# Kernel tuning notes

Hardware: AMD Instinct MI355X
Metric: run time of the kernel (lower is better)

Reference implementation:

```python
import jax, jax.numpy as jnp
import numpy as np

# Config mirrors cfg['cluster'] and point_cloud_range from init_kwargs
PCR = np.array([-51.2, -51.2, -5.0, 51.2, 51.2, 3.0], dtype=np.float32)
VOXEL_SIZE = 0.2
SIZE_X = 512  # floor((51.2 - (-51.2)) / 0.2)
EPS = 1.5
MIN_SAMPLES = 5
MIN_P_CLUSTER = 20


def _cluster(points):
    """Faithful jax version of Cluster.forward for batch_size == 1.

    voxel_down_sample -> DBSCAN (euclidean, eps, min_samples) on voxel coords
    -> drop clusters with < MIN_P_CLUSTER voxels -> scatter labels back to points.
    """
    N = points.shape[0]
    # --- voxel_down_sample ---
    coords = jnp.floor((points[:, 1:3] - PCR[:2]) / VOXEL_SIZE).astype(jnp.int32)  # (N,2) x,y
    merged = coords[:, 1] * SIZE_X + coords[:, 0]
    # static-size unique: padded entries get fill_value=-1 at the end
    uniq, inv = jnp.unique(merged, size=N, fill_value=-1, return_inverse=True)
    valid = uniq >= 0  # (N,) real voxels
    vox = jnp.stack([uniq % SIZE_X, uniq // SIZE_X], axis=1).astype(jnp.float32)  # (N,2)

    # --- DBSCAN on voxel coords ---
    d2 = jnp.sum((vox[:, None, :] - vox[None, :, :]) ** 2, axis=-1)  # (N,N)
    adj = (d2 <= EPS * EPS) & valid[:, None] & valid[None, :]  # includes self-edge
    core = (jnp.sum(adj, axis=1) >= MIN_SAMPLES) & valid  # sklearn counts self

    BIG = N  # sentinel > any label
    labels0 = jnp.where(core, jnp.arange(N), BIG)
    adj_core = adj & core[None, :]

    def min_core_neighbor(labels):
        return jnp.min(jnp.where(adj_core, labels[None, :], BIG), axis=1)

    def body(carry):
        labels, _ = carry
        new = jnp.where(core, jnp.minimum(labels, min_core_neighbor(labels)), labels)
        return new, jnp.any(new != labels)

    # min-label propagation = connected components over core-core eps graph
    labels, _ = jax.lax.while_loop(lambda c: c[1], body, (labels0, jnp.array(True)))

    # border points attach to a neighboring core cluster; otherwise noise (-1)
    nb = min_core_neighbor(labels)
    raw = jnp.where(core, labels, jnp.where(valid & (nb < BIG), nb, -1))  # root-id or -1

    # relabel root-ids to consecutive 0..k-1 (sklearn numbering by smallest core idx)
    roots = jnp.unique(raw, size=N, fill_value=BIG)  # sorted; BIG padding at end
    pos = jnp.searchsorted(roots, raw)
    dense = pos - (roots[0] == -1).astype(pos.dtype)
    dense = jnp.where(raw >= 0, dense, -1)

    # drop small clusters (by voxel count), keep remaining ids unchanged
    counts = jnp.zeros(N, jnp.int32).at[jnp.where(dense >= 0, dense, 0)].add(
        jnp.where(dense >= 0, 1, 0))
    keep = counts >= MIN_P_CLUSTER
    final = jnp.where((dense >= 0) & keep[jnp.clip(dense, 0, N - 1)], dense, -1)

    # scatter voxel labels back to points (points_inst_idx has points.dtype, like torch)
    pts_inst = final[inv].astype(points.dtype)
    max_num_inst = jnp.maximum(jnp.max(final) + 1, 0)
    return pts_inst, max_num_inst


def setup_inputs() -> dict:
    key = jax.random.key(0)
    N = 8192
    k1, k2, k3, k4, k5, k6, k7 = jax.random.split(key, 7)
    n_blobs = 64
    centers = jax.random.uniform(k1, (n_blobs, 2), minval=-48.0, maxval=48.0)
    assign = jax.random.randint(k2, (N,), 0, n_blobs)
    xy = centers[assign] + jax.random.normal(k3, (N, 2)) * 1.0
    noise = jax.random.uniform(k4, (N,)) < 0.2
    xy = jnp.where(noise[:, None], jax.random.uniform(k5, (N, 2), minval=-51.0, maxval=51.0), xy)
    xy = jnp.clip(xy, -51.0, 51.0)
    z = jax.random.uniform(k6, (N, 1), minval=-3.0, maxval=1.0)
    feat = jax.random.normal(k7, (N, 1))
    points = jnp.concatenate([jnp.zeros((N, 1)), xy, z, feat], axis=1).astype(jnp.float32)
    return {"points": points, "batch_size": 1}


def reference(points, batch_size):
    # voxel_down_sample asserts batch_size == 1; single-batch path.
    return _cluster(points)
```

## Files before the change

kernel.cpp:

```cpp
#include <hip/hip_runtime.h>
#include <stdint.h>


#define GRIDW 512
#define WPR 16
#define NWORDS 8192
#define NCELLS 262144
#define NONE 0xFFFFFFFFu

#define OFF_OCC    0
#define OFF_ROOTBM 8192
#define OFF_KEEPBM 16384
#define OFF_RPRE   24576
#define OFF_LAB    32768
#define OFF_CNT    294912

__device__ __forceinline__ void hsum(uint32_t l, uint32_t c, uint32_t r,
                                     uint32_t& h0, uint32_t& h1) {
  uint32_t Wb = (c << 1) | (l >> 31);
  uint32_t Eb = (c >> 1) | (r << 31);
  h0 = Wb ^ c ^ Eb;
  h1 = (Wb & c) | (Eb & (Wb ^ c));
}

__device__ __forceinline__ uint32_t ge5(uint32_t a0, uint32_t a1, uint32_t b0,
                                        uint32_t b1, uint32_t c0, uint32_t c1) {
  uint32_t u0 = a0 ^ b0, cy = a0 & b0;
  uint32_t t = a1 ^ b1;
  uint32_t u1 = t ^ cy;
  uint32_t u2 = (a1 & b1) | (cy & t);
  uint32_t v0 = u0 ^ c0, k0 = u0 & c0;
  uint32_t t2 = u1 ^ c1;
  uint32_t v1 = t2 ^ k0;
  uint32_t k1 = (u1 & c1) | (k0 & t2);
  uint32_t v2 = u2 ^ k1;
  uint32_t v3 = u2 & k1;
  return v3 | (v2 & (v1 | v0));
}

__device__ __forceinline__ uint32_t coreRbit(uint32_t cU, uint32_t rU, uint32_t cM,
                                             uint32_t rM, uint32_t cD, uint32_t rD) {
  if (!(rM & 1u)) return 0u;
  int n = __popc((cU >> 31) | ((rU & 3u) << 1)) +
          __popc((cM >> 31) | ((rM & 3u) << 1)) +
          __popc((cD >> 31) | ((rD & 3u) << 1));
  return n >= 5 ? 1u : 0u;
}

__device__ __forceinline__ uint32_t coreLbit(uint32_t cU, uint32_t lU, uint32_t cM,
                                             uint32_t lM, uint32_t cD, uint32_t lD) {
  if (!(lM >> 31)) return 0u;
  int n = __popc(((lU >> 30) & 3u) | ((cU & 1u) << 2)) +
          __popc(((lM >> 30) & 3u) | ((cM & 1u) << 2)) +
          __popc(((lD >> 30) & 3u) | ((cD & 1u) << 2));
  return n >= 5 ? 1u : 0u;
}

__device__ __forceinline__ uint32_t aread(uint32_t* p) {
  return __hip_atomic_load(p, __ATOMIC_RELAXED, __HIP_MEMORY_SCOPE_AGENT);
}

__device__ __forceinline__ uint32_t findc(uint32_t* L, uint32_t x) {
  uint32_t r = x, p = aread(&L[r]);
  while (p != r) { r = p; p = aread(&L[r]); }
  while (x > r) {
    uint32_t nx = aread(&L[x]);
    if (nx <= r) break;
    atomicCAS(&L[x], nx, r);
    x = nx;
  }
  return r;
}

__device__ __forceinline__ void unite(uint32_t* L, uint32_t a, uint32_t b) {
  for (;;) {
    a = findc(L, a);
    b = findc(L, b);
    if (a == b) return;
    uint32_t lo = min(a, b), hi = max(a, b);
    if (atomicCAS(&L[hi], hi, lo) == hi) return;
    a = lo; b = hi;
  }
}

__global__ void k_init(uint32_t* __restrict__ ws) {
  int i = blockIdx.x * 256 + threadIdx.x;
  ws[OFF_LAB + i] = (uint32_t)i;
  ws[OFF_CNT + i] = 0u;
  if (i < NWORDS) { ws[OFF_OCC + i] = 0u; ws[OFF_ROOTBM + i] = 0u; }
}

__global__ void k_vox(const float* __restrict__ pts, uint32_t* __restrict__ ws,
                      int npts) {
  int i = blockIdx.x * 256 + threadIdx.x;
  if (i >= npts) return;
  float x = pts[i * 5 + 1];
  float y = pts[i * 5 + 2];
  int cx = (int)floorf((x - (-51.2f)) / 0.2f);
  int cy = (int)floorf((y - (-51.2f)) / 0.2f);
  cx = min(max(cx, 0), GRIDW - 1);
  cy = min(max(cy, 0), GRIDW - 1);
  int cell = cy * GRIDW + cx;
  atomicOr(&ws[OFF_OCC + (cell >> 5)], 1u << (cell & 31));
}

__global__ void k_merge(uint32_t* __restrict__ ws) {
  int cell = blockIdx.x * 256 + threadIdx.x;
  const uint32_t* occ = ws + OFF_OCC;
  uint32_t* lab = ws + OFF_LAB;
  int wi = cell >> 5, b = cell & 31, wx = wi & 15, y = cell >> 9;
  uint32_t cB = occ[wi];
  if (!((cB >> b) & 1)) return;
  uint32_t lB = wx ? occ[wi - 1] : 0u;
  uint32_t rB = (wx < 15) ? occ[wi + 1] : 0u;
  uint32_t cA = 0, lA = 0, rA = 0, cC = 0, lC = 0, rC = 0, cD = 0, lD = 0, rD = 0;
  if (y > 0) { int w = wi - WPR; cA = occ[w]; lA = wx ? occ[w - 1] : 0u; rA = (wx < 15) ? occ[w + 1] : 0u; }
  if (y < GRIDW - 1) { int w = wi + WPR; cC = occ[w]; lC = wx ? occ[w - 1] : 0u; rC = (wx < 15) ? occ[w + 1] : 0u; }
  if (y < GRIDW - 2) { int w = wi + 2 * WPR; cD = occ[w]; lD = wx ? occ[w - 1] : 0u; rD = (wx < 15) ? occ[w + 1] : 0u; }
  uint32_t hA0, hA1, hB0, hB1, hC0, hC1, hD0, hD1;
  hsum(lA, cA, rA, hA0, hA1); hsum(lB, cB, rB, hB0, hB1);
  hsum(lC, cC, rC, hC0, hC1); hsum(lD, cD, rD, hD0, hD1);
  uint32_t cmB = ge5(hA0, hA1, hB0, hB1, hC0, hC1) & cB;
  if (!((cmB >> b) & 1)) return;
  bool eC = (b < 31) ? (((cmB >> (b + 1)) & 1) != 0)
                     : (coreRbit(cA, rA, cB, rB, cC, rC) != 0);
  if (eC) unite(lab, cell, cell + 1);
  if (y < GRIDW - 1) {
    uint32_t cmS = ge5(hB0, hB1, hC0, hC1, hD0, hD1) & cC;
    if ((cmS >> b) & 1) unite(lab, cell, cell + GRIDW);
    bool seC = (b < 31) ? (((cmS >> (b + 1)) & 1) != 0)
                        : (coreRbit(cB, rB, cC, rC, cD, rD) != 0);
    if (seC) unite(lab, cell, cell + GRIDW + 1);
    bool swC = (b > 0) ? (((cmS >> (b - 1)) & 1) != 0)
                       : (coreLbit(cB, lB, cC, lC, cD, lD) != 0);
    if (swC) unite(lab, cell, cell + GRIDW - 1);
  }
}

__global__ void k_cb(uint32_t* __restrict__ ws) {
  int cell = blockIdx.x * 256 + threadIdx.x;
  const uint32_t* occ = ws + OFF_OCC;
  uint32_t* lab = ws + OFF_LAB;
  uint32_t* cnt = ws + OFF_CNT;
  int wi = cell >> 5, b = cell & 31, wx = wi & 15, y = cell >> 9;
  uint32_t cB = occ[wi];
  if (!((cB >> b) & 1)) return;
  uint32_t lB = wx ? occ[wi - 1] : 0u;
  uint32_t rB = (wx < 15) ? occ[wi + 1] : 0u;
  uint32_t cZ = 0, lZ = 0, rZ = 0, cA = 0, lA = 0, rA = 0;
  uint32_t cC = 0, lC = 0, rC = 0, cD = 0, lD = 0, rD = 0;
  if (y > 1) { int w = wi - 2 * WPR; cZ = occ[w]; lZ = wx ? occ[w - 1] : 0u; rZ = (wx < 15) ? occ[w + 1] : 0u; }
  if (y > 0) { int w = wi - WPR; cA = occ[w]; lA = wx ? occ[w - 1] : 0u; rA = (wx < 15) ? occ[w + 1] : 0u; }
  if (y < GRIDW - 1) { int w = wi + WPR; cC = occ[w]; lC = wx ? occ[w - 1] : 0u; rC = (wx < 15) ? occ[w + 1] : 0u; }
  if (y < GRIDW - 2) { int w = wi + 2 * WPR; cD = occ[w]; lD = wx ? occ[w - 1] : 0u; rD = (wx < 15) ? occ[w + 1] : 0u; }
  uint32_t hZ0, hZ1, hA0, hA1, hB0, hB1, hC0, hC1, hD0, hD1;
  hsum(lZ, cZ, rZ, hZ0, hZ1); hsum(lA, cA, rA, hA0, hA1); hsum(lB, cB, rB, hB0, hB1);
  hsum(lC, cC, rC, hC0, hC1); hsum(lD, cD, rD, hD0, hD1);
  uint32_t cw0 = ge5(hA0, hA1, hB0, hB1, hC0, hC1) & cB;
  if ((cw0 >> b) & 1) {
    uint32_t root = findc(lab, cell);
    lab[cell] = root;
    if (root == (uint32_t)cell) atomicOr(&ws[OFF_ROOTBM + wi], 1u << b);
    atomicAdd(&cnt[root], 1u);
  } else {
    uint32_t cwm1 = ge5(hZ0, hZ1, hA0, hA1, hB0, hB1) & cA;
    uint32_t cw1 = ge5(hB0, hB1, hC0, hC1, hD0, hD1) & cC;
    uint32_t m = NONE;
    bool t;
    t = (b > 0) ? (((cw0 >> (b - 1)) & 1) != 0) : (coreLbit(cA, lA, cB, lB, cC, lC) != 0);
    if (t) m = min(m, findc(lab, cell - 1));
    t = (b < 31) ? (((cw0 >> (b + 1)) & 1) != 0) : (coreRbit(cA, rA, cB, rB, cC, rC) != 0);
    if (t) m = min(m, findc(lab, cell + 1));
    if (y > 0) {
      if ((cwm1 >> b) & 1) m = min(m, findc(lab, cell - GRIDW));
      t = (b > 0) ? (((cwm1 >> (b - 1)) & 1) != 0) : (coreLbit(cZ, lZ, cA, lA, cB, lB) != 0);
      if (t) m = min(m, findc(lab, cell - GRIDW - 1));
      t = (b < 31) ? (((cwm1 >> (b + 1)) & 1) != 0) : (coreRbit(cZ, rZ, cA, rA, cB, rB) != 0);
      if (t) m = min(m, findc(lab, cell - GRIDW + 1));
    }
    if (y < GRIDW - 1) {
      if ((cw1 >> b) & 1) m = min(m, findc(lab, cell + GRIDW));
      t = (b > 0) ? (((cw1 >> (b - 1)) & 1) != 0) : (coreLbit(cB, lB, cC, lC, cD, lD) != 0);
      if (t) m = min(m, findc(lab, cell + GRIDW - 1));
      t = (b < 31) ? (((cw1 >> (b + 1)) & 1) != 0) : (coreRbit(cB, rB, cC, rC, cD, rD) != 0);
      if (t) m = min(m, findc(lab, cell + GRIDW + 1));
    }
    lab[cell] = m;
    if (m != NONE) atomicAdd(&cnt[m], 1u);
  }
}

__global__ void k_finish(uint32_t* __restrict__ ws, float* __restrict__ out,
                         int npts) {
  __shared__ uint32_t wsum[4];
  __shared__ int smax;
  int tid = threadIdx.x;
  if (tid == 0) smax = -1;
  int base = tid * 32;
  uint32_t s = 0;
  for (int j = 0; j < 32; j++) s += __popc(ws[OFF_ROOTBM + base + j]);
  int lane = tid & 63, wv = tid >> 6;
  uint32_t inc = s;
  for (int d = 1; d < 64; d <<= 1) { uint32_t t = __shfl_up(inc, d); if (lane >= d) inc += t; }
  if (lane == 63) wsum[wv] = inc;
  __syncthreads();
  uint32_t woff = 0;
  for (int k = 0; k < wv; k++) woff += wsum[k];
  uint32_t excl = woff + inc - s;
  int mx = -1;
  for (int j = 0; j < 32; j++) {
    uint32_t rbw = ws[OFF_ROOTBM + base + j];
    ws[OFF_RPRE + base + j] = excl;
    uint32_t rb = rbw, keep = 0;
    int d = (int)excl;
    while (rb) {
      int b2 = __ffs(rb) - 1; rb &= rb - 1;
      int r = (base + j) * 32 + b2;
      if (ws[OFF_CNT + r] >= 20u) { keep |= 1u << b2; mx = d; }
      d++;
    }
    ws[OFF_KEEPBM + base + j] = keep;
    excl += __popc(rbw);
  }
  if (mx >= 0) atomicMax(&smax, mx);
  __syncthreads();
  if (tid == 0) out[npts] = (float)(smax + 1);
}

__global__ void k_scatter(const float* __restrict__ pts,
                          const uint32_t* __restrict__ ws,
                          float* __restrict__ out, int npts) {
  int i = blockIdx.x * 256 + threadIdx.x;
  if (i >= npts) return;
  float x = pts[i * 5 + 1];
  float y = pts[i * 5 + 2];
  int cx = (int)floorf((x - (-51.2f)) / 0.2f);
  int cy = (int)floorf((y - (-51.2f)) / 0.2f);
  cx = min(max(cx, 0), GRIDW - 1);
  cy = min(max(cy, 0), GRIDW - 1);
  int cell = cy * GRIDW + cx;
  uint32_t l = ws[OFF_LAB + cell];
  float o = -1.0f;
  if (l != NONE) {
    if ((ws[OFF_KEEPBM + (l >> 5)] >> (l & 31)) & 1) {
      int dnum = ws[OFF_RPRE + (l >> 5)] +
                 __popc(ws[OFF_ROOTBM + (l >> 5)] & ((1u << (l & 31)) - 1u));
      o = (float)dnum;
    }
  }
  out[i] = o;
}

extern "C" void kernel_launch(void* const* d_in, const int* in_sizes, int n_in,
                              void* d_out, int out_size, void* d_ws, size_t ws_size,
                              hipStream_t stream) {
  const float* pts = (const float*)d_in[0];
  int npts = in_sizes[0] / 5;
  uint32_t* ws = (uint32_t*)d_ws;
  float* out = (float*)d_out;
  int pblocks = (npts + 255) / 256;
  k_init<<<NCELLS / 256, 256, 0, stream>>>(ws);
  k_vox<<<pblocks, 256, 0, stream>>>(pts, ws, npts);
  k_merge<<<NCELLS / 256, 256, 0, stream>>>(ws);
  k_cb<<<NCELLS / 256, 256, 0, stream>>>(ws);
  k_finish<<<1, 256, 0, stream>>>(ws, out, npts);
  k_scatter<<<pblocks, 256, 0, stream>>>(pts, ws, out, npts);
}
```

Measured before the change: 113.7 us.

## Build a compact worklist of occupied voxels and drop the full-grid init kernel

Voxelization now appends each newly occupied cell to a compact worklist and lazily initializes that cell's label and count. This replaces the full-grid init kernel with a small memset of the occupancy bitmap, root bitmap and worklist counter. The merge and core/border kernels launch a fixed 32 blocks over the worklist instead of one thread per grid cell, and fetch the extra neighbor rows (Z and D) only on the branches that need them. This removes dense-grid traffic and idle threads. The fixed 32×256 grid assumes at most 8192 occupied cells, and worklist order is no longer spatial, so memory access becomes less coalesced.

```diff
diff --git a/kernel.cpp b/kernel.cpp
--- a/kernel.cpp
+++ b/kernel.cpp
@@ -5,15 +5,17 @@
 #define GRIDW 512
 #define WPR 16
 #define NWORDS 8192
-#define NCELLS 262144
 #define NONE 0xFFFFFFFFu
 
 #define OFF_OCC    0
 #define OFF_ROOTBM 8192
-#define OFF_KEEPBM 16384
-#define OFF_RPRE   24576
-#define OFF_LAB    32768
-#define OFF_CNT    294912
+#define OFF_NOCC   16384
+#define FILL_BYTES ((16384 + 1) * 4)
+#define OFF_WL     16448
+#define OFF_KEEPBM 24640
+#define OFF_RPRE   32832
+#define OFF_LAB    41024
+#define OFF_CNT    303168
 
 __device__ __forceinline__ void hsum(uint32_t l, uint32_t c, uint32_t r,
                                      uint32_t& h0, uint32_t& h1) {
@@ -83,13 +85,6 @@
   }
 }
 
-__global__ void k_init(uint32_t* __restrict__ ws) {
-  int i = blockIdx.x * 256 + threadIdx.x;
-  ws[OFF_LAB + i] = (uint32_t)i;
-  ws[OFF_CNT + i] = 0u;
-  if (i < NWORDS) { ws[OFF_OCC + i] = 0u; ws[OFF_ROOTBM + i] = 0u; }
-}
-
 __global__ void k_vox(const float* __restrict__ pts, uint32_t* __restrict__ ws,
                       int npts) {
   int i = blockIdx.x * 256 + threadIdx.x;
@@ -101,31 +96,40 @@
   cx = min(max(cx, 0), GRIDW - 1);
   cy = min(max(cy, 0), GRIDW - 1);
   int cell = cy * GRIDW + cx;
-  atomicOr(&ws[OFF_OCC + (cell >> 5)], 1u << (cell & 31));
+  uint32_t old = atomicOr(&ws[OFF_OCC + (cell >> 5)], 1u << (cell & 31));
+  if (!((old >> (cell & 31)) & 1)) {
+    uint32_t idx = atomicAdd(&ws[OFF_NOCC], 1u);
+    ws[OFF_WL + idx] = (uint32_t)cell;
+    ws[OFF_LAB + cell] = (uint32_t)cell;
+    ws[OFF_CNT + cell] = 0u;
+  }
 }
 
 __global__ void k_merge(uint32_t* __restrict__ ws) {
-  int cell = blockIdx.x * 256 + threadIdx.x;
+  int i = blockIdx.x * 256 + threadIdx.x;
+  if (i >= (int)ws[OFF_NOCC]) return;
+  int cell = (int)ws[OFF_WL + i];
   const uint32_t* occ = ws + OFF_OCC;
   uint32_t* lab = ws + OFF_LAB;
   int wi = cell >> 5, b = cell & 31, wx = wi & 15, y = cell >> 9;
   uint32_t cB = occ[wi];
-  if (!((cB >> b) & 1)) return;
   uint32_t lB = wx ? occ[wi - 1] : 0u;
   uint32_t rB = (wx < 15) ? occ[wi + 1] : 0u;
-  uint32_t cA = 0, lA = 0, rA = 0, cC = 0, lC = 0, rC = 0, cD = 0, lD = 0, rD = 0;
+  uint32_t cA = 0, lA = 0, rA = 0, cC = 0, lC = 0, rC = 0;
   if (y > 0) { int w = wi - WPR; cA = occ[w]; lA = wx ? occ[w - 1] : 0u; rA = (wx < 15) ? occ[w + 1] : 0u; }
   if (y < GRIDW - 1) { int w = wi + WPR; cC = occ[w]; lC = wx ? occ[w - 1] : 0u; rC = (wx < 15) ? occ[w + 1] : 0u; }
-  if (y < GRIDW - 2) { int w = wi + 2 * WPR; cD = occ[w]; lD = wx ? occ[w - 1] : 0u; rD = (wx < 15) ? occ[w + 1] : 0u; }
-  uint32_t hA0, hA1, hB0, hB1, hC0, hC1, hD0, hD1;
-  hsum(lA, cA, rA, hA0, hA1); hsum(lB, cB, rB, hB0, hB1);
-  hsum(lC, cC, rC, hC0, hC1); hsum(lD, cD, rD, hD0, hD1);
+  uint32_t hA0, hA1, hB0, hB1, hC0, hC1;
+  hsum(lA, cA, rA, hA0, hA1); hsum(lB, cB, rB, hB0, hB1); hsum(lC, cC, rC, hC0, hC1);
   uint32_t cmB = ge5(hA0, hA1, hB0, hB1, hC0, hC1) & cB;
   if (!((cmB >> b) & 1)) return;
   bool eC = (b < 31) ? (((cmB >> (b + 1)) & 1) != 0)
                      : (coreRbit(cA, rA, cB, rB, cC, rC) != 0);
   if (eC) unite(lab, cell, cell + 1);
   if (y < GRIDW - 1) {
+    uint32_t cD = 0, lD = 0, rD = 0;
+    if (y < GRIDW - 2) { int w = wi + 2 * WPR; cD = occ[w]; lD = wx ? occ[w - 1] : 0u; rD = (wx < 15) ? occ[w + 1] : 0u; }
+    uint32_t hD0, hD1;
+    hsum(lD, cD, rD, hD0, hD1);
     uint32_t cmS = ge5(hB0, hB1, hC0, hC1, hD0, hD1) & cC;
     if ((cmS >> b) & 1) unite(lab, cell, cell + GRIDW);
     bool seC = (b < 31) ? (((cmS >> (b + 1)) & 1) != 0)
@@ -138,24 +142,21 @@
 }
 
 __global__ void k_cb(uint32_t* __restrict__ ws) {
-  int cell = blockIdx.x * 256 + threadIdx.x;
+  int i = blockIdx.x * 256 + threadIdx.x;
+  if (i >= (int)ws[OFF_NOCC]) return;
+  int cell = (int)ws[OFF_WL + i];
   const uint32_t* occ = ws + OFF_OCC;
   uint32_t* lab = ws + OFF_LAB;
   uint32_t* cnt = ws + OFF_CNT;
   int wi = cell >> 5, b = cell & 31, wx = wi & 15, y = cell >> 9;
   uint32_t cB = occ[wi];
-  if (!((cB >> b) & 1)) return;
   uint32_t lB = wx ? occ[wi - 1] : 0u;
   uint32_t rB = (wx < 15) ? occ[wi + 1] : 0u;
-  uint32_t cZ = 0, lZ = 0, rZ = 0, cA = 0, lA = 0, rA = 0;
-  uint32_t cC = 0, lC = 0, rC = 0, cD = 0, lD = 0, rD = 0;
-  if (y > 1) { int w = wi - 2 * WPR; cZ = occ[w]; lZ = wx ? occ[w - 1] : 0u; rZ = (wx < 15) ? occ[w + 1] : 0u; }
+  uint32_t cA = 0, lA = 0, rA = 0, cC = 0, lC = 0, rC = 0;
   if (y > 0) { int w = wi - WPR; cA = occ[w]; lA = wx ? occ[w - 1] : 0u; rA = (wx < 15) ? occ[w + 1] : 0u; }
   if (y < GRIDW - 1) { int w = wi + WPR; cC = occ[w]; lC = wx ? occ[w - 1] : 0u; rC = (wx < 15) ? occ[w + 1] : 0u; }
-  if (y < GRIDW - 2) { int w = wi + 2 * WPR; cD = occ[w]; lD = wx ? occ[w - 1] : 0u; rD = (wx < 15) ? occ[w + 1] : 0u; }
-  uint32_t hZ0, hZ1, hA0, hA1, hB0, hB1, hC0, hC1, hD0, hD1;
-  hsum(lZ, cZ, rZ, hZ0, hZ1); hsum(lA, cA, rA, hA0, hA1); hsum(lB, cB, rB, hB0, hB1);
-  hsum(lC, cC, rC, hC0, hC1); hsum(lD, cD, rD, hD0, hD1);
+  uint32_t hA0, hA1, hB0, hB1, hC0, hC1;
+  hsum(lA, cA, rA, hA0, hA1); hsum(lB, cB, rB, hB0, hB1); hsum(lC, cC, rC, hC0, hC1);
   uint32_t cw0 = ge5(hA0, hA1, hB0, hB1, hC0, hC1) & cB;
   if ((cw0 >> b) & 1) {
     uint32_t root = findc(lab, cell);
@@ -163,8 +164,6 @@
     if (root == (uint32_t)cell) atomicOr(&ws[OFF_ROOTBM + wi], 1u << b);
     atomicAdd(&cnt[root], 1u);
   } else {
-    uint32_t cwm1 = ge5(hZ0, hZ1, hA0, hA1, hB0, hB1) & cA;
-    uint32_t cw1 = ge5(hB0, hB1, hC0, hC1, hD0, hD1) & cC;
     uint32_t m = NONE;
     bool t;
     t = (b > 0) ? (((cw0 >> (b - 1)) & 1) != 0) : (coreLbit(cA, lA, cB, lB, cC, lC) != 0);
@@ -172,6 +171,11 @@
     t = (b < 31) ? (((cw0 >> (b + 1)) & 1) != 0) : (coreRbit(cA, rA, cB, rB, cC, rC) != 0);
     if (t) m = min(m, findc(lab, cell + 1));
     if (y > 0) {
+      uint32_t cZ = 0, lZ = 0, rZ = 0;
+      if (y > 1) { int w = wi - 2 * WPR; cZ = occ[w]; lZ = wx ? occ[w - 1] : 0u; rZ = (wx < 15) ? occ[w + 1] : 0u; }
+      uint32_t hZ0, hZ1;
+      hsum(lZ, cZ, rZ, hZ0, hZ1);
+      uint32_t cwm1 = ge5(hZ0, hZ1, hA0, hA1, hB0, hB1) & cA;
       if ((cwm1 >> b) & 1) m = min(m, findc(lab, cell - GRIDW));
       t = (b > 0) ? (((cwm1 >> (b - 1)) & 1) != 0) : (coreLbit(cZ, lZ, cA, lA, cB, lB) != 0);
       if (t) m = min(m, findc(lab, cell - GRIDW - 1));
@@ -179,6 +183,11 @@
       if (t) m = min(m, findc(lab, cell - GRIDW + 1));
     }
     if (y < GRIDW - 1) {
+      uint32_t cD = 0, lD = 0, rD = 0;
+      if (y < GRIDW - 2) { int w = wi + 2 * WPR; cD = occ[w]; lD = wx ? occ[w - 1] : 0u; rD = (wx < 15) ? occ[w + 1] : 0u; }
+      uint32_t hD0, hD1;
+      hsum(lD, cD, rD, hD0, hD1);
+      uint32_t cw1 = ge5(hB0, hB1, hC0, hC1, hD0, hD1) & cC;
       if ((cw1 >> b) & 1) m = min(m, findc(lab, cell + GRIDW));
       t = (b > 0) ? (((cw1 >> (b - 1)) & 1) != 0) : (coreLbit(cB, lB, cC, lC, cD, lD) != 0);
       if (t) m = min(m, findc(lab, cell + GRIDW - 1));
@@ -241,12 +250,10 @@
   int cell = cy * GRIDW + cx;
   uint32_t l = ws[OFF_LAB + cell];
   float o = -1.0f;
-  if (l != NONE) {
-    if ((ws[OFF_KEEPBM + (l >> 5)] >> (l & 31)) & 1) {
-      int dnum = ws[OFF_RPRE + (l >> 5)] +
-                 __popc(ws[OFF_ROOTBM + (l >> 5)] & ((1u << (l & 31)) - 1u));
-      o = (float)dnum;
-    }
+  if (l != NONE && ((ws[OFF_KEEPBM + (l >> 5)] >> (l & 31)) & 1)) {
+    int dnum = ws[OFF_RPRE + (l >> 5)] +
+               __popc(ws[OFF_ROOTBM + (l >> 5)] & ((1u << (l & 31)) - 1u));
+    o = (float)dnum;
   }
   out[i] = o;
 }
@@ -259,10 +266,10 @@
   uint32_t* ws = (uint32_t*)d_ws;
   float* out = (float*)d_out;
   int pblocks = (npts + 255) / 256;
-  k_init<<<NCELLS / 256, 256, 0, stream>>>(ws);
+  hipMemsetAsync(d_ws, 0, FILL_BYTES, stream);
   k_vox<<<pblocks, 256, 0, stream>>>(pts, ws, npts);
-  k_merge<<<NCELLS / 256, 256, 0, stream>>>(ws);
-  k_cb<<<NCELLS / 256, 256, 0, stream>>>(ws);
+  k_merge<<<32, 256, 0, stream>>>(ws);
+  k_cb<<<32, 256, 0, stream>>>(ws);
   k_finish<<<1, 256, 0, stream>>>(ws, out, npts);
   k_scatter<<<pblocks, 256, 0, stream>>>(pts, ws, out, npts);
 }
```

Result: slower. 126.9 us (+11.6%).

## Precompute core bitmask, lazy-init labels, fuse finish into scatter

Applied to the files above, without the earlier changes.

Adds a per-word kernel that computes the core-point bitmask once, so the merge and border kernels read it instead of recomputing neighbour-count bit sums. Replaces the full-grid init kernel with a small memset of the occupancy words, and initializes labels and counts only for cells that k_vox newly sets. Fuses the single-block finish kernel into the scatter kernel: every scatter block redundantly recomputes the root prefix sums and keep bitmask in shared memory, which removes one launch but duplicates that scan work across blocks.

```diff
diff --git a/kernel.cpp b/kernel.cpp
--- a/kernel.cpp
+++ b/kernel.cpp
@@ -10,10 +10,10 @@
 
 #define OFF_OCC    0
 #define OFF_ROOTBM 8192
-#define OFF_KEEPBM 16384
-#define OFF_RPRE   24576
-#define OFF_LAB    32768
-#define OFF_CNT    294912
+#define OFF_CM     16384
+#define OFF_LAB    24576
+#define OFF_CNT    286720
+#define FILL_BYTES (NWORDS * 4)
 
 __device__ __forceinline__ void hsum(uint32_t l, uint32_t c, uint32_t r,
                                      uint32_t& h0, uint32_t& h1) {
@@ -38,24 +38,6 @@
   return v3 | (v2 & (v1 | v0));
 }
 
-__device__ __forceinline__ uint32_t coreRbit(uint32_t cU, uint32_t rU, uint32_t cM,
-                                             uint32_t rM, uint32_t cD, uint32_t rD) {
-  if (!(rM & 1u)) return 0u;
-  int n = __popc((cU >> 31) | ((rU & 3u) << 1)) +
-          __popc((cM >> 31) | ((rM & 3u) << 1)) +
-          __popc((cD >> 31) | ((rD & 3u) << 1));
-  return n >= 5 ? 1u : 0u;
-}
-
-__device__ __forceinline__ uint32_t coreLbit(uint32_t cU, uint32_t lU, uint32_t cM,
-                                             uint32_t lM, uint32_t cD, uint32_t lD) {
-  if (!(lM >> 31)) return 0u;
-  int n = __popc(((lU >> 30) & 3u) | ((cU & 1u) << 2)) +
-          __popc(((lM >> 30) & 3u) | ((cM & 1u) << 2)) +
-          __popc(((lD >> 30) & 3u) | ((cD & 1u) << 2));
-  return n >= 5 ? 1u : 0u;
-}
-
 __device__ __forceinline__ uint32_t aread(uint32_t* p) {
   return __hip_atomic_load(p, __ATOMIC_RELAXED, __HIP_MEMORY_SCOPE_AGENT);
 }
@@ -81,13 +63,6 @@
     if (atomicCAS(&L[hi], hi, lo) == hi) return;
     a = lo; b = hi;
   }
-}
-
-__global__ void k_init(uint32_t* __restrict__ ws) {
-  int i = blockIdx.x * 256 + threadIdx.x;
-  ws[OFF_LAB + i] = (uint32_t)i;
-  ws[OFF_CNT + i] = 0u;
-  if (i < NWORDS) { ws[OFF_OCC + i] = 0u; ws[OFF_ROOTBM + i] = 0u; }
 }
 
 __global__ void k_vox(const float* __restrict__ pts, uint32_t* __restrict__ ws,
@@ -101,38 +76,47 @@
   cx = min(max(cx, 0), GRIDW - 1);
   cy = min(max(cy, 0), GRIDW - 1);
   int cell = cy * GRIDW + cx;
-  atomicOr(&ws[OFF_OCC + (cell >> 5)], 1u << (cell & 31));
+  uint32_t old = atomicOr(&ws[OFF_OCC + (cell >> 5)], 1u << (cell & 31));
+  if (!((old >> (cell & 31)) & 1)) {
+    ws[OFF_LAB + cell] = (uint32_t)cell;
+    ws[OFF_CNT + cell] = 0u;
+  }
+}
+
+__global__ void k_cm(uint32_t* __restrict__ ws) {
+  int wi = blockIdx.x * 256 + threadIdx.x;
+  const uint32_t* occ = ws + OFF_OCC;
+  ws[OFF_ROOTBM + wi] = 0u;
+  uint32_t cB = occ[wi];
+  int y = wi >> 4, wx = wi & 15;
+  uint32_t lB = wx ? occ[wi - 1] : 0u;
+  uint32_t rB = (wx < 15) ? occ[wi + 1] : 0u;
+  uint32_t cA = 0, lA = 0, rA = 0, cC = 0, lC = 0, rC = 0;
+  if (y > 0) { int w = wi - WPR; cA = occ[w]; lA = wx ? occ[w - 1] : 0u; rA = (wx < 15) ? occ[w + 1] : 0u; }
+  if (y < GRIDW - 1) { int w = wi + WPR; cC = occ[w]; lC = wx ? occ[w - 1] : 0u; rC = (wx < 15) ? occ[w + 1] : 0u; }
+  uint32_t a0, a1, b0, b1, c0, c1;
+  hsum(lA, cA, rA, a0, a1); hsum(lB, cB, rB, b0, b1); hsum(lC, cC, rC, c0, c1);
+  ws[OFF_CM + wi] = ge5(a0, a1, b0, b1, c0, c1) & cB;
 }
 
 __global__ void k_merge(uint32_t* __restrict__ ws) {
   int cell = blockIdx.x * 256 + threadIdx.x;
-  const uint32_t* occ = ws + OFF_OCC;
+  const uint32_t* cm = ws + OFF_CM;
   uint32_t* lab = ws + OFF_LAB;
   int wi = cell >> 5, b = cell & 31, wx = wi & 15, y = cell >> 9;
-  uint32_t cB = occ[wi];
-  if (!((cB >> b) & 1)) return;
-  uint32_t lB = wx ? occ[wi - 1] : 0u;
-  uint32_t rB = (wx < 15) ? occ[wi + 1] : 0u;
-  uint32_t cA = 0, lA = 0, rA = 0, cC = 0, lC = 0, rC = 0, cD = 0, lD = 0, rD = 0;
-  if (y > 0) { int w = wi - WPR; cA = occ[w]; lA = wx ? occ[w - 1] : 0u; rA = (wx < 15) ? occ[w + 1] : 0u; }
-  if (y < GRIDW - 1) { int w = wi + WPR; cC = occ[w]; lC = wx ? occ[w - 1] : 0u; rC = (wx < 15) ? occ[w + 1] : 0u; }
-  if (y < GRIDW - 2) { int w = wi + 2 * WPR; cD = occ[w]; lD = wx ? occ[w - 1] : 0u; rD = (wx < 15) ? occ[w + 1] : 0u; }
-  uint32_t hA0, hA1, hB0, hB1, hC0, hC1, hD0, hD1;
-  hsum(lA, cA, rA, hA0, hA1); hsum(lB, cB, rB, hB0, hB1);
-  hsum(lC, cC, rC, hC0, hC1); hsum(lD, cD, rD, hD0, hD1);
-  uint32_t cmB = ge5(hA0, hA1, hB0, hB1, hC0, hC1) & cB;
-  if (!((cmB >> b) & 1)) return;
-  bool eC = (b < 31) ? (((cmB >> (b + 1)) & 1) != 0)
-                     : (coreRbit(cA, rA, cB, rB, cC, rC) != 0);
+  uint32_t cw0 = cm[wi];
+  if (!((cw0 >> b) & 1)) return;
+  bool eC = (b < 31) ? (((cw0 >> (b + 1)) & 1) != 0)
+                     : ((wx < 15) ? ((cm[wi + 1] & 1u) != 0) : false);
   if (eC) unite(lab, cell, cell + 1);
   if (y < GRIDW - 1) {
-    uint32_t cmS = ge5(hB0, hB1, hC0, hC1, hD0, hD1) & cC;
+    uint32_t cmS = cm[wi + WPR];
     if ((cmS >> b) & 1) unite(lab, cell, cell + GRIDW);
     bool seC = (b < 31) ? (((cmS >> (b + 1)) & 1) != 0)
-                        : (coreRbit(cB, rB, cC, rC, cD, rD) != 0);
+                        : ((wx < 15) ? ((cm[wi + WPR + 1] & 1u) != 0) : false);
     if (seC) unite(lab, cell, cell + GRIDW + 1);
     bool swC = (b > 0) ? (((cmS >> (b - 1)) & 1) != 0)
-                       : (coreLbit(cB, lB, cC, lC, cD, lD) != 0);
+                       : ((wx > 0) ? ((cm[wi + WPR - 1] >> 31) != 0) : false);
     if (swC) unite(lab, cell, cell + GRIDW - 1);
   }
 }
@@ -140,49 +124,44 @@
 __global__ void k_cb(uint32_t* __restrict__ ws) {
   int cell = blockIdx.x * 256 + threadIdx.x;
   const uint32_t* occ = ws + OFF_OCC;
+  const uint32_t* cm = ws + OFF_CM;
   uint32_t* lab = ws + OFF_LAB;
   uint32_t* cnt = ws + OFF_CNT;
   int wi = cell >> 5, b = cell & 31, wx = wi & 15, y = cell >> 9;
-  uint32_t cB = occ[wi];
-  if (!((cB >> b) & 1)) return;
-  uint32_t lB = wx ? occ[wi - 1] : 0u;
-  uint32_t rB = (wx < 15) ? occ[wi + 1] : 0u;
-  uint32_t cZ = 0, lZ = 0, rZ = 0, cA = 0, lA = 0, rA = 0;
-  uint32_t cC = 0, lC = 0, rC = 0, cD = 0, lD = 0, rD = 0;
-  if (y > 1) { int w = wi - 2 * WPR; cZ = occ[w]; lZ = wx ? occ[w - 1] : 0u; rZ = (wx < 15) ? occ[w + 1] : 0u; }
-  if (y > 0) { int w = wi - WPR; cA = occ[w]; lA = wx ? occ[w - 1] : 0u; rA = (wx < 15) ? occ[w + 1] : 0u; }
-  if (y < GRIDW - 1) { int w = wi + WPR; cC = occ[w]; lC = wx ? occ[w - 1] : 0u; rC = (wx < 15) ? occ[w + 1] : 0u; }
-  if (y < GRIDW - 2) { int w = wi + 2 * WPR; cD = occ[w]; lD = wx ? occ[w - 1] : 0u; rD = (wx < 15) ? occ[w + 1] : 0u; }
-  uint32_t hZ0, hZ1, hA0, hA1, hB0, hB1, hC0, hC1, hD0, hD1;
-  hsum(lZ, cZ, rZ, hZ0, hZ1); hsum(lA, cA, rA, hA0, hA1); hsum(lB, cB, rB, hB0, hB1);
-  hsum(lC, cC, rC, hC0, hC1); hsum(lD, cD, rD, hD0, hD1);
-  uint32_t cw0 = ge5(hA0, hA1, hB0, hB1, hC0, hC1) & cB;
+  if (!((occ[wi] >> b) & 1)) return;
+  uint32_t cw0 = cm[wi];
   if ((cw0 >> b) & 1) {
     uint32_t root = findc(lab, cell);
     lab[cell] = root;
     if (root == (uint32_t)cell) atomicOr(&ws[OFF_ROOTBM + wi], 1u << b);
     atomicAdd(&cnt[root], 1u);
   } else {
-    uint32_t cwm1 = ge5(hZ0, hZ1, hA0, hA1, hB0, hB1) & cA;
-    uint32_t cw1 = ge5(hB0, hB1, hC0, hC1, hD0, hD1) & cC;
     uint32_t m = NONE;
     bool t;
-    t = (b > 0) ? (((cw0 >> (b - 1)) & 1) != 0) : (coreLbit(cA, lA, cB, lB, cC, lC) != 0);
+    t = (b > 0) ? (((cw0 >> (b - 1)) & 1) != 0)
+                : ((wx > 0) ? ((cm[wi - 1] >> 31) != 0) : false);
     if (t) m = min(m, findc(lab, cell - 1));
-    t = (b < 31) ? (((cw0 >> (b + 1)) & 1) != 0) : (coreRbit(cA, rA, cB, rB, cC, rC) != 0);
+    t = (b < 31) ? (((cw0 >> (b + 1)) & 1) != 0)
+                 : ((wx < 15) ? ((cm[wi + 1] & 1u) != 0) : false);
     if (t) m = min(m, findc(lab, cell + 1));
     if (y > 0) {
-      if ((cwm1 >> b) & 1) m = min(m, findc(lab, cell - GRIDW));
-      t = (b > 0) ? (((cwm1 >> (b - 1)) & 1) != 0) : (coreLbit(cZ, lZ, cA, lA, cB, lB) != 0);
+      uint32_t cmN = cm[wi - WPR];
+      if ((cmN >> b) & 1) m = min(m, findc(lab, cell - GRIDW));
+      t = (b > 0) ? (((cmN >> (b - 1)) & 1) != 0)
+                  : ((wx > 0) ? ((cm[wi - WPR - 1] >> 31) != 0) : false);
       if (t) m = min(m, findc(lab, cell - GRIDW - 1));
-      t = (b < 31) ? (((cwm1 >> (b + 1)) & 1) != 0) : (coreRbit(cZ, rZ, cA, rA, cB, rB) != 0);
+      t = (b < 31) ? (((cmN >> (b + 1)) & 1) != 0)
+                   : ((wx < 15) ? ((cm[wi - WPR + 1] & 1u) != 0) : false);
       if (t) m = min(m, findc(lab, cell - GRIDW + 1));
     }
     if (y < GRIDW - 1) {
-      if ((cw1 >> b) & 1) m = min(m, findc(lab, cell + GRIDW));
-      t = (b > 0) ? (((cw1 >> (b - 1)) & 1) != 0) : (coreLbit(cB, lB, cC, lC, cD, lD) != 0);
+      uint32_t cmS = cm[wi + WPR];
+      if ((cmS >> b) & 1) m = min(m, findc(lab, cell + GRIDW));
+      t = (b > 0) ? (((cmS >> (b - 1)) & 1) != 0)
+                  : ((wx > 0) ? ((cm[wi + WPR - 1] >> 31) != 0) : false);
       if (t) m = min(m, findc(lab, cell + GRIDW - 1));
-      t = (b < 31) ? (((cw1 >> (b + 1)) & 1) != 0) : (coreRbit(cB, rB, cC, rC, cD, rD) != 0);
+      t = (b < 31) ? (((cmS >> (b + 1)) & 1) != 0)
+                   : ((wx < 15) ? ((cm[wi + WPR + 1] & 1u) != 0) : false);
       if (t) m = min(m, findc(lab, cell + GRIDW + 1));
     }
     lab[cell] = m;
@@ -190,8 +169,11 @@
   }
 }
 
-__global__ void k_finish(uint32_t* __restrict__ ws, float* __restrict__ out,
-                         int npts) {
+__global__ __launch_bounds__(256) void k_scatter(
+    const float* __restrict__ pts, uint32_t* __restrict__ ws,
+    float* __restrict__ out, int npts) {
+  __shared__ uint32_t rpre_s[NWORDS];
+  __shared__ uint32_t keep_s[NWORDS];
   __shared__ uint32_t wsum[4];
   __shared__ int smax;
   int tid = threadIdx.x;
@@ -210,7 +192,7 @@
   int mx = -1;
   for (int j = 0; j < 32; j++) {
     uint32_t rbw = ws[OFF_ROOTBM + base + j];
-    ws[OFF_RPRE + base + j] = excl;
+    rpre_s[base + j] = excl;
     uint32_t rb = rbw, keep = 0;
     int d = (int)excl;
     while (rb) {
@@ -219,36 +201,30 @@
       if (ws[OFF_CNT + r] >= 20u) { keep |= 1u << b2; mx = d; }
       d++;
     }
-    ws[OFF_KEEPBM + base + j] = keep;
+    keep_s[base + j] = keep;
     excl += __popc(rbw);
   }
   if (mx >= 0) atomicMax(&smax, mx);
   __syncthreads();
-  if (tid == 0) out[npts] = (float)(smax + 1);
-}
-
-__global__ void k_scatter(const float* __restrict__ pts,
-                          const uint32_t* __restrict__ ws,
-                          float* __restrict__ out, int npts) {
-  int i = blockIdx.x * 256 + threadIdx.x;
-  if (i >= npts) return;
-  float x = pts[i * 5 + 1];
-  float y = pts[i * 5 + 2];
-  int cx = (int)floorf((x - (-51.2f)) / 0.2f);
-  int cy = (int)floorf((y - (-51.2f)) / 0.2f);
-  cx = min(max(cx, 0), GRIDW - 1);
-  cy = min(max(cy, 0), GRIDW - 1);
-  int cell = cy * GRIDW + cx;
-  uint32_t l = ws[OFF_LAB + cell];
-  float o = -1.0f;
-  if (l != NONE) {
-    if ((ws[OFF_KEEPBM + (l >> 5)] >> (l & 31)) & 1) {
-      int dnum = ws[OFF_RPRE + (l >> 5)] +
+  int i = blockIdx.x * 256 + tid;
+  if (i < npts) {
+    float x = pts[i * 5 + 1];
+    float y = pts[i * 5 + 2];
+    int cx = (int)floorf((x - (-51.2f)) / 0.2f);
+    int cy = (int)floorf((y - (-51.2f)) / 0.2f);
+    cx = min(max(cx, 0), GRIDW - 1);
+    cy = min(max(cy, 0), GRIDW - 1);
+    int cell = cy * GRIDW + cx;
+    uint32_t l = ws[OFF_LAB + cell];
+    float o = -1.0f;
+    if (l != NONE && ((keep_s[l >> 5] >> (l & 31)) & 1)) {
+      int dnum = rpre_s[l >> 5] +
                  __popc(ws[OFF_ROOTBM + (l >> 5)] & ((1u << (l & 31)) - 1u));
       o = (float)dnum;
     }
-  }
-  out[i] = o;
+    out[i] = o;
+  }
+  if (tid == 0) out[npts] = (float)(smax + 1);
 }
 
 extern "C" void kernel_launch(void* const* d_in, const int* in_sizes, int n_in,
@@ -259,10 +235,10 @@
   uint32_t* ws = (uint32_t*)d_ws;
   float* out = (float*)d_out;
   int pblocks = (npts + 255) / 256;
-  k_init<<<NCELLS / 256, 256, 0, stream>>>(ws);
+  hipMemsetAsync(d_ws, 0, FILL_BYTES, stream);
   k_vox<<<pblocks, 256, 0, stream>>>(pts, ws, npts);
+  k_cm<<<NWORDS / 256, 256, 0, stream>>>(ws);
   k_merge<<<NCELLS / 256, 256, 0, stream>>>(ws);
   k_cb<<<NCELLS / 256, 256, 0, stream>>>(ws);
-  k_finish<<<1, 256, 0, stream>>>(ws, out, npts);
   k_scatter<<<pblocks, 256, 0, stream>>>(pts, ws, out, npts);
 }
```

Measured after the change: 104.3 us. -8.3%, faster.
